# Optimization experiments

Measured on AMD Instinct MI355X. Metric: run time of the kernel, lower is better.

## Reference

```python
import jax, jax.numpy as jnp
import numpy as np

# 5G NR LDPC BG1-like parameters
Z = 384          # lifting factor
MB, NB = 46, 68  # basegraph rows / cols (BG1)
DEG = 7          # check-node base degree (~316/46 edges of real BG1)
K = 8448         # info bits (= k_ldpc = 22*Z, no filler bits)
N = 25344        # transmitted bits = n_ldpc - 2*Z (rate 1/3)
N_LDPC = NB * Z  # 26112 variable nodes
M = MB * Z       # 17664 check nodes
E = MB * DEG * Z # 123648 edges
NUM_ITER = 20
LLR_MAX = 20.0
BATCH = 128


def _build_graph():
    """Deterministic lifted quasi-cyclic Tanner graph (BG1-like)."""
    rng = np.random.default_rng(0)
    rows, cols = [], []
    i = np.arange(Z)
    for r in range(MB):
        cs = rng.choice(NB, DEG, replace=False)
        for c in cs:
            shift = int(rng.integers(Z))
            rows.append(r * Z + i)
            cols.append(c * Z + (i + shift) % Z)
    return (np.concatenate(rows).astype(np.int32),
            np.concatenate(cols).astype(np.int32))


def setup_inputs() -> dict:
    key = jax.random.key(0)
    row, col = _build_graph()
    llr_ch = 4.0 * jax.random.normal(key, (BATCH, N), dtype=jnp.float32)
    return {"llr_ch": llr_ch, "row": jnp.asarray(row), "col": jnp.asarray(col)}


def _decode(llr_ch, row, col):
    """5G rate recovery + flooding min-sum BP, soft info-bit LLR output."""
    B = llr_ch.shape[0]
    llr = jnp.clip(llr_ch, -LLR_MAX, LLR_MAX)
    # de-rate-matching: first 2*Z systematic bits are punctured -> LLR 0
    llr_full = jnp.concatenate([jnp.zeros((B, 2 * Z), llr.dtype), llr], axis=1)
    # Sionna LLR convention log p(1)/p(0): negate for internal BP
    lch = -llr_full.T                       # [N_LDPC, B]
    eid = jnp.arange(E)
    inf = jnp.asarray(1e9, lch.dtype)
    m_cv0 = jnp.zeros((E, B), lch.dtype)

    def step(m_cv, _):
        # ---- VN update (extrinsic) ----
        vn_sum = lch + jax.ops.segment_sum(m_cv, col, num_segments=N_LDPC)
        m_vc = vn_sum[col] - m_cv           # [E, B]
        # ---- CN update: min-sum with exclude-self min ----
        mag = jnp.abs(m_vc)
        neg = m_vc < 0
        min1 = jax.ops.segment_min(mag, row, num_segments=M)       # [M, B]
        is_min = mag <= min1[row]
        cand = jnp.where(is_min, eid[:, None], E)
        first = jax.ops.segment_min(cand, row, num_segments=M)     # first argmin
        is_the_min = eid[:, None] == first[row]
        min2 = jax.ops.segment_min(jnp.where(is_the_min, inf, mag),
                                   row, num_segments=M)
        out_mag = jnp.where(is_the_min, min2[row], min1[row])
        n_neg = jax.ops.segment_sum(neg.astype(jnp.int32), row, num_segments=M)
        sign_tot = (1 - 2 * (n_neg % 2))[row].astype(mag.dtype)
        sign_excl = sign_tot * jnp.where(neg, -1.0, 1.0)           # s_tot / s_e
        return sign_excl * out_mag, None

    m_cv, _ = jax.lax.scan(step, m_cv0, None, length=NUM_ITER)
    x_tot = lch + jax.ops.segment_sum(m_cv, col, num_segments=N_LDPC)
    llr_out = -x_tot.T                      # back to p(1)/p(0) convention
    return llr_out[:, :K]                   # systematic info-bit LLRs


def reference(llr_ch, row, col):
    return _decode(llr_ch, row, col)
```

## Files before the change

### kernel.cpp

```cpp
#include <hip/hip_runtime.h>

#define Zl      384
#define MBr     46
#define NBc     68
#define DEG     7
#define K_INFO  8448
#define N_TX    25344
#define N_LDPC  (NBc * Zl)
#define M_CHK   (MBr * Zl)
#define E_EDGE  (MBr * DEG * Zl)
#define BATCH   128
#define NUM_ITER 20
#define LLR_MAXF 20.0f
#define BCAP    32



__global__ void prep_kernel(const float* __restrict__ llr, float* __restrict__ lch) {
    __shared__ float tile[32][33];
    const int n0 = blockIdx.x * 32, b0 = blockIdx.y * 32;
    const int tx = threadIdx.x, ty = threadIdx.y;
#pragma unroll
    for (int j = 0; j < 4; ++j) {
        float v = llr[(b0 + ty + 8 * j) * N_TX + n0 + tx];
        v = fminf(fmaxf(v, -LLR_MAXF), LLR_MAXF);
        tile[ty + 8 * j][tx] = -v;
    }
    __syncthreads();
#pragma unroll
    for (int j = 0; j < 4; ++j) {
        const int b = b0 + tx;
        const int n = n0 + ty + 8 * j;
        lch[((size_t)(b >> 3) * N_LDPC + 2 * Zl + n) * 8 + (b & 7)] = tile[tx][ty + 8 * j];
    }
}

__global__ void base_build_kernel(const int* __restrict__ col,
                                  int* __restrict__ bcount, int* __restrict__ badj,
                                  int* __restrict__ cadj) {
    __shared__ int sc[MBr * DEG];
    __shared__ int ssh[MBr * DEG];
    const int t = threadIdx.x;
    if (t < MBr * DEG) {
        const int v0 = col[t * Zl];
        const int c  = v0 / Zl;
        sc[t]  = c;
        ssh[t] = v0 - c * Zl;
        cadj[t] = ssh[t] | (sc[t] << 10);
    }
    if (t < NBc) bcount[t] = 0;
    __syncthreads();
    if (t < MBr * DEG) {
        const int c = sc[t];
        int slot = 0;
        for (int u = 0; u < t; ++u) slot += (sc[u] == c) ? 1 : 0;
        const int r = t / DEG, d = t - r * DEG;
        if (slot < BCAP) badj[c * BCAP + slot] = ssh[t] | (d << 10) | (r << 13);
        atomicAdd(&bcount[c], 1);
    }
}

template <bool FIRST>
__global__ void cn_kernel(const float* __restrict__ x,
                          float* __restrict__ state_f2,
                          unsigned short* __restrict__ meta,
                          const int* __restrict__ cadj, const int h) {
    const int qg   = blockIdx.x & 7;
    const int tile = blockIdx.x >> 3;
    const int nl   = threadIdx.x >> 1;
    const int ql   = threadIdx.x & 1;
    const int s    = h * 8 + qg;
    const int cn   = tile * 128 + nl;
    const int r    = cn / Zl;
    const int i    = cn - r * Zl;

    const float4* xp = (const float4*)x + (size_t)s * N_LDPC * 2;
    float4* sp = (float4*)state_f2 + ((size_t)s * M_CHK + cn) * 4 + ql * 2;
    ushort4* mp = (ushort4*)meta + ((size_t)s * M_CHK + cn) * 2 + ql;

    float omin1[4], omin2[4];
    int oamin[4]; unsigned onm[4], ostot[4];
    if (!FIRST) {
        const float4 sA = sp[0];
        const float4 sB = sp[1];
        omin1[0] = sA.x; omin2[0] = sA.y; omin1[1] = sA.z; omin2[1] = sA.w;
        omin1[2] = sB.x; omin2[2] = sB.y; omin1[3] = sB.z; omin2[3] = sB.w;
        const ushort4 mt = mp[0];
        const unsigned m4[4] = {mt.x, mt.y, mt.z, mt.w};
#pragma unroll
        for (int c = 0; c < 4; ++c) {
            oamin[c] = m4[c] & 7u;
            onm[c]   = (m4[c] >> 3) & 0x7Fu;
            ostot[c] = (m4[c] >> 10) & 1u;
        }
    }

    float min1[4] = {1e30f, 1e30f, 1e30f, 1e30f};
    float min2[4] = {1e30f, 1e30f, 1e30f, 1e30f};
    int   amin[4] = {0, 0, 0, 0};
    unsigned nm[4] = {0u, 0u, 0u, 0u};

#pragma unroll
    for (int d = 0; d < DEG; ++d) {
        const int pk = cadj[r * DEG + d];
        const int sh = pk & 0x3FF;
        const int c  = pk >> 10;
        int ii = i + sh; if (ii >= Zl) ii -= Zl;
        const int v = c * Zl + ii;
        const float4 xv = xp[(size_t)v * 2 + ql];
        float t[4] = {xv.x, xv.y, xv.z, xv.w};
        if (!FIRST) {
#pragma unroll
            for (int c2 = 0; c2 < 4; ++c2) {
                const float omag = (d == oamin[c2]) ? omin2[c2] : omin1[c2];
                const float mold = (ostot[c2] ^ ((onm[c2] >> d) & 1u)) ? -omag : omag;
                t[c2] -= mold;
            }
        }
#pragma unroll
        for (int c2 = 0; c2 < 4; ++c2) {
            const float mag = fabsf(t[c2]);
            nm[c2] |= (t[c2] < 0.f ? 1u : 0u) << d;
            if (mag < min1[c2]) { min2[c2] = min1[c2]; min1[c2] = mag; amin[c2] = d; }
            else if (mag < min2[c2]) { min2[c2] = mag; }
        }
    }

    float4 oA, oB;
    oA.x = min1[0]; oA.y = min2[0]; oA.z = min1[1]; oA.w = min2[1];
    oB.x = min1[2]; oB.y = min2[2]; oB.z = min1[3]; oB.w = min2[3];
    sp[0] = oA;
    sp[1] = oB;
    ushort4 mo;
    unsigned mv[4];
#pragma unroll
    for (int c = 0; c < 4; ++c)
        mv[c] = (unsigned)amin[c] | (nm[c] << 3) | ((unsigned)(__popc(nm[c]) & 1) << 10);
    mo.x = (unsigned short)mv[0]; mo.y = (unsigned short)mv[1];
    mo.z = (unsigned short)mv[2]; mo.w = (unsigned short)mv[3];
    mp[0] = mo;
}

__global__ void vn_kernel(const float* __restrict__ lch,
                          const float* __restrict__ state_f2,
                          const unsigned short* __restrict__ meta,
                          const int* __restrict__ bcount, const int* __restrict__ badj,
                          float* __restrict__ x, const int h) {
    const int qg   = blockIdx.x & 7;
    const int tile = blockIdx.x >> 3;
    const int nl   = threadIdx.x >> 1;
    const int ql   = threadIdx.x & 1;
    const int s    = h * 8 + qg;
    const int v    = tile * 128 + nl;
    const int c    = v / Zl;
    const int j    = v - c * Zl;
    const int cnt  = min(bcount[c], BCAP);
    const int* bp  = badj + c * BCAP;
    const float4* stp = (const float4*)state_f2 + (size_t)s * M_CHK * 4;
    const ushort4* mtp = (const ushort4*)meta + (size_t)s * M_CHK * 2;

    float4 sacc = ((const float4*)lch)[((size_t)s * N_LDPC + v) * 2 + ql];
    for (int k = 0; k < cnt; ++k) {
        const int pk = bp[k];
        const int sh = pk & 0x3FF;
        const int d  = (pk >> 10) & 7;
        const int r  = pk >> 13;
        int i = j - sh;
        if (i < 0) i += Zl;
        const int cnb = r * Zl + i;
        const float4 sA = stp[(size_t)cnb * 4 + ql * 2];
        const float4 sB = stp[(size_t)cnb * 4 + ql * 2 + 1];
        const ushort4 mt = mtp[(size_t)cnb * 2 + ql];
        const unsigned m4[4] = {mt.x, mt.y, mt.z, mt.w};
        const float mn1[4] = {sA.x, sA.z, sB.x, sB.z};
        const float mn2[4] = {sA.y, sA.w, sB.y, sB.w};
        float val[4];
#pragma unroll
        for (int cc = 0; cc < 4; ++cc) {
            const int   am  = m4[cc] & 7u;
            const unsigned nmv = (m4[cc] >> 3) & 0x7Fu;
            const unsigned st  = (m4[cc] >> 10) & 1u;
            const float mag = (d == am) ? mn2[cc] : mn1[cc];
            val[cc] = (st ^ ((nmv >> d) & 1u)) ? -mag : mag;
        }
        sacc.x += val[0]; sacc.y += val[1]; sacc.z += val[2]; sacc.w += val[3];
    }
    ((float4*)x)[((size_t)s * N_LDPC + v) * 2 + ql] = sacc;
}

__global__ void out_kernel(const float* __restrict__ x, float* __restrict__ out) {
    __shared__ float tile[32][33];
    const int k0 = blockIdx.x * 32, b0 = blockIdx.y * 32;
    const int tx = threadIdx.x, ty = threadIdx.y;
#pragma unroll
    for (int j = 0; j < 4; ++j) {
        const int b = b0 + tx;
        const int k = k0 + ty + 8 * j;
        tile[ty + 8 * j][tx] = -x[((size_t)(b >> 3) * N_LDPC + k) * 8 + (b & 7)];
    }
    __syncthreads();
#pragma unroll
    for (int j = 0; j < 4; ++j) {
        out[(b0 + ty + 8 * j) * K_INFO + k0 + tx] = tile[tx][ty + 8 * j];
    }
}

extern "C" void kernel_launch(void* const* d_in, const int* in_sizes, int n_in,
                              void* d_out, int out_size, void* d_ws, size_t ws_size,
                              hipStream_t stream) {
    const float* llr = (const float*)d_in[0];
    const int* col = (const int*)d_in[2];
    float* out = (float*)d_out;

    char* ws = (char*)d_ws;
    float* lch   = (float*)ws;
    float* x     = lch + (size_t)N_LDPC * BATCH;
    float* state = x + (size_t)N_LDPC * BATCH;
    unsigned short* meta = (unsigned short*)(state + (size_t)M_CHK * BATCH * 2);
    int* bcount = (int*)(meta + (size_t)M_CHK * BATCH);
    int* badj   = bcount + NBc;
    int* cadj   = badj + NBc * BCAP;

    hipMemsetAsync(lch, 0, (size_t)N_LDPC * BATCH * sizeof(float), stream);
    prep_kernel<<<dim3(N_TX / 32, BATCH / 32), dim3(32, 8), 0, stream>>>(llr, lch);

    base_build_kernel<<<1, 512, 0, stream>>>(col, bcount, badj, cadj);

    const int cn_grid = (M_CHK / 128) * 8;
    const int vn_grid = (N_LDPC / 128) * 8;

    for (int h = 0; h < 2; ++h) {
        cn_kernel<true><<<cn_grid, 256, 0, stream>>>(lch, state, meta, cadj, h);
        vn_kernel<<<vn_grid, 256, 0, stream>>>(lch, state, meta, bcount, badj, x, h);
        for (int t = 1; t < NUM_ITER; ++t) {
            cn_kernel<false><<<cn_grid, 256, 0, stream>>>(x, state, meta, cadj, h);
            vn_kernel<<<vn_grid, 256, 0, stream>>>(lch, state, meta, bcount, badj, x, h);
        }
    }

    out_kernel<<<dim3(K_INFO / 32, BATCH / 32), dim3(32, 8), 0, stream>>>(x, out);
}
```

Baseline: 699.6 us.

## Fuse CN/VN iteration launches into persistent kernel with per-group grid barriers

Replaces the 80 separate CN and VN kernel launches with a single persistent kernel. It uses 552 blocks in 8 independent groups of 69, one group per 8-sample slice. Each group synchronises with a software grid barrier built on atomic counter and generation words between the CN and VN phases. The aim is to remove launch overhead and inter-kernel drain gaps. The risks are deadlock if not all blocks are co-resident, barrier spin cost, and fewer blocks covering the tiles.

```diff
diff --git a/kernel.cpp b/kernel.cpp
--- a/kernel.cpp
+++ b/kernel.cpp
@@ -14,6 +14,11 @@
 #define LLR_MAXF 20.0f
 #define BCAP    32
 
+#define NPG      69
+#define NBLK     (NPG * 8)
+#define CN_TILES (M_CHK / 128)
+#define VN_TILES (N_LDPC / 128)
+
 
 
 __global__ void prep_kernel(const float* __restrict__ llr, float* __restrict__ lch) {
@@ -60,21 +65,34 @@
     }
 }
 
+__device__ __forceinline__ void gsync(unsigned* cnt, unsigned* gen) {
+    __syncthreads();
+    if (threadIdx.x == 0) {
+        const unsigned g0 = __hip_atomic_load(gen, __ATOMIC_RELAXED, __HIP_MEMORY_SCOPE_AGENT);
+        const unsigned old = __hip_atomic_fetch_add(cnt, 1u, __ATOMIC_RELAXED, __HIP_MEMORY_SCOPE_AGENT);
+        if (old == (unsigned)(NPG - 1)) {
+            __hip_atomic_store(cnt, 0u, __ATOMIC_RELAXED, __HIP_MEMORY_SCOPE_AGENT);
+            asm volatile("s_waitcnt vmcnt(0)" ::: "memory");
+            __hip_atomic_store(gen, g0 + 1u, __ATOMIC_RELAXED, __HIP_MEMORY_SCOPE_AGENT);
+        } else {
+            while (__hip_atomic_load(gen, __ATOMIC_RELAXED, __HIP_MEMORY_SCOPE_AGENT) == g0)
+                __builtin_amdgcn_s_sleep(2);
+        }
+        asm volatile("buffer_inv sc0\n\ts_waitcnt vmcnt(0)" ::: "memory");
+    }
+    __syncthreads();
+}
+
 template <bool FIRST>
-__global__ void cn_kernel(const float* __restrict__ x,
-                          float* __restrict__ state_f2,
-                          unsigned short* __restrict__ meta,
-                          const int* __restrict__ cadj, const int h) {
-    const int qg   = blockIdx.x & 7;
-    const int tile = blockIdx.x >> 3;
-    const int nl   = threadIdx.x >> 1;
-    const int ql   = threadIdx.x & 1;
-    const int s    = h * 8 + qg;
-    const int cn   = tile * 128 + nl;
-    const int r    = cn / Zl;
-    const int i    = cn - r * Zl;
-
-    const float4* xp = (const float4*)x + (size_t)s * N_LDPC * 2;
+__device__ __forceinline__ void cn_tile(const float* __restrict__ xin,
+                                        float* __restrict__ state_f2,
+                                        unsigned short* __restrict__ meta,
+                                        const int* __restrict__ cadj,
+                                        const int s, const int cn, const int ql) {
+    const int r = cn / Zl;
+    const int i = cn - r * Zl;
+
+    const float4* xp = (const float4*)xin + (size_t)s * N_LDPC * 2;
     float4* sp = (float4*)state_f2 + ((size_t)s * M_CHK + cn) * 4 + ql * 2;
     ushort4* mp = (ushort4*)meta + ((size_t)s * M_CHK + cn) * 2 + ql;
 
@@ -141,21 +159,17 @@
     mp[0] = mo;
 }
 
-__global__ void vn_kernel(const float* __restrict__ lch,
-                          const float* __restrict__ state_f2,
-                          const unsigned short* __restrict__ meta,
-                          const int* __restrict__ bcount, const int* __restrict__ badj,
-                          float* __restrict__ x, const int h) {
-    const int qg   = blockIdx.x & 7;
-    const int tile = blockIdx.x >> 3;
-    const int nl   = threadIdx.x >> 1;
-    const int ql   = threadIdx.x & 1;
-    const int s    = h * 8 + qg;
-    const int v    = tile * 128 + nl;
-    const int c    = v / Zl;
-    const int j    = v - c * Zl;
-    const int cnt  = min(bcount[c], BCAP);
-    const int* bp  = badj + c * BCAP;
+__device__ __forceinline__ void vn_tile(const float* __restrict__ lch,
+                                        const float* __restrict__ state_f2,
+                                        const unsigned short* __restrict__ meta,
+                                        const int* __restrict__ bcount,
+                                        const int* __restrict__ badj,
+                                        float* __restrict__ x,
+                                        const int s, const int v, const int ql) {
+    const int c = v / Zl;
+    const int j = v - c * Zl;
+    const int cnt = min(bcount[c], BCAP);
+    const int* bp = badj + c * BCAP;
     const float4* stp = (const float4*)state_f2 + (size_t)s * M_CHK * 4;
     const ushort4* mtp = (const ushort4*)meta + (size_t)s * M_CHK * 2;
 
@@ -188,6 +202,36 @@
     ((float4*)x)[((size_t)s * N_LDPC + v) * 2 + ql] = sacc;
 }
 
+__global__ void __launch_bounds__(256, 4)
+decode_persist(const float* __restrict__ lch, float* __restrict__ x,
+               float* __restrict__ state, unsigned short* __restrict__ meta,
+               const int* __restrict__ bcount, const int* __restrict__ badj,
+               const int* __restrict__ cadj, unsigned* __restrict__ bar) {
+    const int g  = blockIdx.x & 7;
+    const int bg = blockIdx.x >> 3;
+    const int nl = threadIdx.x >> 1;
+    const int ql = threadIdx.x & 1;
+    unsigned* cnt = bar + (size_t)g * 64;
+    unsigned* gen = bar + (size_t)g * 64 + 32;
+
+    for (int h = 0; h < 2; ++h) {
+        const int s = h * 8 + g;
+        for (int t = 0; t < NUM_ITER; ++t) {
+            if (t == 0) {
+                cn_tile<true>(lch, state, meta, cadj, s, bg * 128 + nl, ql);
+                cn_tile<true>(lch, state, meta, cadj, s, (bg + NPG) * 128 + nl, ql);
+            } else {
+                cn_tile<false>(x, state, meta, cadj, s, bg * 128 + nl, ql);
+                cn_tile<false>(x, state, meta, cadj, s, (bg + NPG) * 128 + nl, ql);
+            }
+            gsync(cnt, gen);
+            for (int tile = bg; tile < VN_TILES; tile += NPG)
+                vn_tile(lch, state, meta, bcount, badj, x, s, tile * 128 + nl, ql);
+            if (t != NUM_ITER - 1) gsync(cnt, gen);
+        }
+    }
+}
+
 __global__ void out_kernel(const float* __restrict__ x, float* __restrict__ out) {
     __shared__ float tile[32][33];
     const int k0 = blockIdx.x * 32, b0 = blockIdx.y * 32;
@@ -220,23 +264,18 @@
     int* bcount = (int*)(meta + (size_t)M_CHK * BATCH);
     int* badj   = bcount + NBc;
     int* cadj   = badj + NBc * BCAP;
+    size_t bar_off = (size_t)((char*)(cadj + 512) - ws);
+    bar_off = (bar_off + 511) & ~(size_t)511;
+    unsigned* bar = (unsigned*)(ws + bar_off);
 
     hipMemsetAsync(lch, 0, (size_t)N_LDPC * BATCH * sizeof(float), stream);
+    hipMemsetAsync(bar, 0, 8 * 64 * sizeof(unsigned), stream);
+
     prep_kernel<<<dim3(N_TX / 32, BATCH / 32), dim3(32, 8), 0, stream>>>(llr, lch);
-
     base_build_kernel<<<1, 512, 0, stream>>>(col, bcount, badj, cadj);
 
-    const int cn_grid = (M_CHK / 128) * 8;
-    const int vn_grid = (N_LDPC / 128) * 8;
-
-    for (int h = 0; h < 2; ++h) {
-        cn_kernel<true><<<cn_grid, 256, 0, stream>>>(lch, state, meta, cadj, h);
-        vn_kernel<<<vn_grid, 256, 0, stream>>>(lch, state, meta, bcount, badj, x, h);
-        for (int t = 1; t < NUM_ITER; ++t) {
-            cn_kernel<false><<<cn_grid, 256, 0, stream>>>(x, state, meta, cadj, h);
-            vn_kernel<<<vn_grid, 256, 0, stream>>>(lch, state, meta, bcount, badj, x, h);
-        }
-    }
+    decode_persist<<<NBLK, 256, 0, stream>>>(lch, x, state, meta,
+                                             bcount, badj, cadj, bar);
 
     out_kernel<<<dim3(K_INFO / 32, BATCH / 32), dim3(32, 8), 0, stream>>>(x, out);
 }
```

Measured after the change: 853.3 us. 22.0% more time.
